# Kernel optimization log

Hardware: AMD Instinct MI355X
Metric: run time of the kernel (lower is better)

Reference implementation:

```python
import jax, jax.numpy as jnp
import numpy as np

L, H, DK, DV, DM, DH = 6, 12, 64, 64, 768, 3072
B, T = 8, 1024


def pos_embed(T, N, dtype):
    pos = jnp.arange(T, dtype=jnp.float32)[:, None]
    i = jnp.arange(N)[None, :]
    exp = ((i // 2) * 2).astype(jnp.float32) / N
    ang = pos / jnp.power(jnp.float32(10000.0), exp)
    pe = jnp.where(i % 2 == 0, jnp.sin(ang), jnp.cos(ang))
    return pe.astype(dtype)


def layernorm(x, g, b, eps=1e-5):
    mu = jnp.mean(x, axis=-1, keepdims=True)
    var = jnp.mean((x - mu) ** 2, axis=-1, keepdims=True)
    return (x - mu) * jax.lax.rsqrt(var + eps) * g + b


def setup_inputs() -> dict:
    key = jax.random.key(0)
    ks = jax.random.split(key, 16)
    s = 0.02
    return {
        "x": jax.random.normal(ks[0], (B, T, DM), dtype=jnp.float32),
        "mask": jnp.ones((B, T), dtype=bool),
        "wq": jax.random.normal(ks[1], (L, H, DM, DK), dtype=jnp.float32) * s,
        "wk": jax.random.normal(ks[2], (L, H, DM, DK), dtype=jnp.float32) * s,
        "wv": jax.random.normal(ks[3], (L, H, DM, DV), dtype=jnp.float32) * s,
        "proj_w": jax.random.normal(ks[4], (L, H * DV, DM), dtype=jnp.float32) * s,
        "proj_b": jnp.zeros((L, DM), dtype=jnp.float32),
        "ln1_g": jnp.ones((L, DM), dtype=jnp.float32),
        "ln1_b": jnp.zeros((L, DM), dtype=jnp.float32),
        "w1": jax.random.normal(ks[5], (L, DM, DH), dtype=jnp.float32) * s,
        "b1": jnp.zeros((L, DH), dtype=jnp.float32),
        "w2": jax.random.normal(ks[6], (L, DH, DM), dtype=jnp.float32) * s,
        "b2": jnp.zeros((L, DM), dtype=jnp.float32),
        "ln2_g": jnp.ones((L, DM), dtype=jnp.float32),
        "ln2_b": jnp.zeros((L, DM), dtype=jnp.float32),
    }


def reference(x, mask, wq, wk, wv, proj_w, proj_b, ln1_g, ln1_b, w1, b1, w2, b2, ln2_g, ln2_b):
    Bx, Tx, Dm = x.shape
    nlayers = wq.shape[0]
    x = x + pos_embed(Tx, Dm, x.dtype)  # sinusoidal PE, added in-place in original
    m = mask[:, None, None, :]          # [B,1,1,Tk], broadcast over heads and queries
    scale = Dm ** 0.5                   # NOTE: original divides by sqrt(Dm), not sqrt(Dk)
    for l in range(nlayers):
        q = jnp.einsum('btd,hdk->bhtk', x, wq[l])
        k = jnp.einsum('bsd,hdk->bhsk', x, wk[l])
        v = jnp.einsum('bsd,hdv->bhsv', x, wv[l])
        attn = jnp.einsum('bhtk,bhsk->bhts', q, k) / scale
        attn = jnp.where(m, attn, -jnp.inf)
        p = jax.nn.softmax(attn, axis=-1)
        o = jnp.einsum('bhts,bhsv->bhtv', p, v)
        o = o.transpose(0, 2, 1, 3).reshape(Bx, Tx, -1)  # concat heads: [B,T,H*Dv]
        o = o @ proj_w[l] + proj_b[l]
        x = layernorm(o + x, ln1_g[l], ln1_b[l])
        h = jax.nn.relu(x @ w1[l] + b1[l])
        f = h @ w2[l] + b2[l]
        x = layernorm(f + x, ln2_g[l], ln2_b[l])
    return x
```

## Files before the change

kernel.cpp:

```cpp
#include <hip/hip_runtime.h>
#include <hip/hip_bf16.h>
#include <math.h>

constexpr int LAYERS = 6;
constexpr int HEADS  = 12;
constexpr int DK     = 64;
constexpr int DM     = 768;
constexpr int DH     = 3072;
constexpr int BATCH  = 8;
constexpr int SEQ    = 1024;
constexpr int MROWS  = BATCH * SEQ;
constexpr float QSCALE = 0.03608439182435161f * 1.4426950408889634f;

typedef __attribute__((ext_vector_type(4))) float f32x4;
typedef __attribute__((ext_vector_type(8))) short bf16x8;
typedef __attribute__((ext_vector_type(4))) unsigned short u16x4;

enum { EPI_QKV = 0, EPI_PROJ = 1, EPI_RELU = 2, EPI_FFN2 = 3 };

__device__ __forceinline__ void gload_lds16(const void* g, void* l) {
  __builtin_amdgcn_global_load_lds(
      (const __attribute__((address_space(1))) void*)g,
      (__attribute__((address_space(3))) void*)l, 16, 0, 0);
}

__global__ __launch_bounds__(256) void posembed_kernel(
    const float* __restrict__ x, __hip_bfloat16* __restrict__ xb) {
  int idx = blockIdx.x * 256 + threadIdx.x;
  int d  = idx % DM;
  int bt = idx / DM;
  int t  = bt & (SEQ - 1);
  float expo = (float)(d & ~1) * (1.0f / (float)DM);
  float inv  = powf(10000.0f, -expo);
  float ang  = (float)t * inv;
  float pe   = (d & 1) ? cosf(ang) : sinf(ang);
  xb[idx] = __float2bfloat16(x[idx] + pe);
}

__global__ __launch_bounds__(256) void transpose_conv(
    const float* __restrict__ in, __hip_bfloat16* __restrict__ out,
    int R, int C, long obatch) {
  __shared__ float tile[32][33];
  int batch = blockIdx.z;
  in  += (long)batch * R * C;
  out += (long)batch * obatch;
  int c0 = blockIdx.x * 32, r0 = blockIdx.y * 32;
  int tx = threadIdx.x, ty = threadIdx.y;
  for (int i = 0; i < 4; i++) {
    int r = r0 + ty + i * 8;
    tile[ty + i * 8][tx] = in[(long)r * C + c0 + tx];
  }
  __syncthreads();
  for (int i = 0; i < 4; i++) {
    int oc = ty + i * 8;
    out[(long)(c0 + oc) * R + r0 + tx] = __float2bfloat16(tile[tx][oc]);
  }
}

__global__ __launch_bounds__(256) void qkv_transpose(
    const float* __restrict__ wq, const float* __restrict__ wk,
    const float* __restrict__ wv, __hip_bfloat16* __restrict__ out) {
  __shared__ float tile[32][33];
  const int z = blockIdx.z;
  const int which = z / 12, head = z % 12;
  const float* in = (which == 0 ? wq : which == 1 ? wk : wv)
                    + (size_t)head * DM * DK;
  __hip_bfloat16* o = out + (size_t)which * DM * DM + (size_t)head * DK * DM;
  int c0 = blockIdx.x * 32, r0 = blockIdx.y * 32;
  int tx = threadIdx.x, ty = threadIdx.y;
  for (int i = 0; i < 4; i++) {
    int r = r0 + ty + i * 8;
    tile[ty + i * 8][tx] = in[(long)r * DK + c0 + tx];
  }
  __syncthreads();
  for (int i = 0; i < 4; i++) {
    int oc = ty + i * 8;
    o[(long)(c0 + oc) * DM + r0 + tx] = __float2bfloat16(tile[tx][oc]);
  }
}

__global__ __launch_bounds__(256) void vtrans_kernel(
    const __hip_bfloat16* __restrict__ v, __hip_bfloat16* __restrict__ vt) {
  __shared__ unsigned short tile[64][66];
  const int head = blockIdx.y;
  const int t0 = blockIdx.x * 64;
  const unsigned short* src =
      (const unsigned short*)v + (size_t)head * SEQ * DK + (size_t)t0 * DK;
  unsigned short* dst = (unsigned short*)vt + (size_t)head * SEQ * DK + t0;
  const int tid = threadIdx.x;
#pragma unroll
  for (int it = 0; it < 4; ++it) {
    int j = tid + it * 256;
    int r = j >> 4;
    int c4 = (j & 15) * 4;
    u16x4 d4 = *(const u16x4*)&src[(size_t)r * DK + c4];
    tile[r][c4 + 0] = d4[0]; tile[r][c4 + 1] = d4[1];
    tile[r][c4 + 2] = d4[2]; tile[r][c4 + 3] = d4[3];
  }
  __syncthreads();
#pragma unroll
  for (int it = 0; it < 4; ++it) {
    int j = tid + it * 256;
    int d = j >> 4;
    int t4 = (j & 15) * 4;
    u16x4 o4;
    o4[0] = tile[t4 + 0][d]; o4[1] = tile[t4 + 1][d];
    o4[2] = tile[t4 + 2][d]; o4[3] = tile[t4 + 3][d];
    *(u16x4*)&dst[(size_t)d * SEQ + t4] = o4;
  }
}

template <int EPI, int BN>
__global__ __launch_bounds__(256, 2) void gemm_bt(
    const __hip_bfloat16* __restrict__ A,
    const __hip_bfloat16* __restrict__ BT,
    int K, int nx,
    const float* __restrict__ bias,
    const __hip_bfloat16* __restrict__ res,
    void* __restrict__ outp) {
  __shared__ __align__(16) char As[2][16384];
  __shared__ __align__(16) char Bs[2][BN * 128];
  constexpr int NF = BN / 32;

  const int nwg = gridDim.x;
  const int cpx = nwg >> 3;
  const int orig = blockIdx.x;
  const int lid = (orig & 7) * cpx + (orig >> 3);
  const int m0 = (lid / nx) * 128;
  const int n0 = (lid % nx) * BN;

  const int tid = threadIdx.x;
  const int lane = tid & 63;
  const int w = tid >> 6;
  const int wm = w >> 1, wn = w & 1;
  const int g = lane >> 4, r16 = lane & 15;
  const int r7 = r16 & 7;

  f32x4 acc[4][NF] = {};

  auto stage = [&](int kt, int d) {
    const int k0 = kt * 64;
#pragma unroll
    for (int i = 0; i < 4; i++) {
      int c = tid + 256 * i;
      int r = c >> 3, cc = (c & 7) ^ (r & 7);
      gload_lds16(&A[(size_t)(m0 + r) * K + k0 + cc * 8], &As[d][c * 16]);
    }
#pragma unroll
    for (int i = 0; i < BN / 32; i++) {
      int c = tid + 256 * i;
      int r = c >> 3, cc = (c & 7) ^ (r & 7);
      gload_lds16(&BT[(size_t)(n0 + r) * K + k0 + cc * 8], &Bs[d][c * 16]);
    }
  };

  const int NT = K >> 6;
  stage(0, 0);
  asm volatile("s_waitcnt vmcnt(0)" ::: "memory");
  __builtin_amdgcn_s_barrier();
  __builtin_amdgcn_sched_barrier(0);

  for (int kt = 0; kt < NT; ++kt) {
    const int cur = kt & 1;
    if (kt + 1 < NT) stage(kt + 1, cur ^ 1);

#pragma unroll
    for (int kk = 0; kk < 2; ++kk) {
      bf16x8 af[4], bfr[NF];
#pragma unroll
      for (int m = 0; m < 4; m++) {
        int R = wm * 64 + m * 16 + r16;
        af[m] = *(const bf16x8*)&As[cur][R * 128 + (((kk * 4 + g) ^ r7) << 4)];
      }
#pragma unroll
      for (int n = 0; n < NF; n++) {
        int R = wn * (BN / 2) + n * 16 + r16;
        bfr[n] = *(const bf16x8*)&Bs[cur][R * 128 + (((kk * 4 + g) ^ r7) << 4)];
      }
      __builtin_amdgcn_s_setprio(1);
#pragma unroll
      for (int m = 0; m < 4; m++)
#pragma unroll
        for (int n = 0; n < NF; n++)
          acc[m][n] = __builtin_amdgcn_mfma_f32_16x16x32_bf16(
              af[m], bfr[n], acc[m][n], 0, 0, 0);
      __builtin_amdgcn_s_setprio(0);
    }

    asm volatile("s_waitcnt vmcnt(0)" ::: "memory");
    __builtin_amdgcn_s_barrier();
    __builtin_amdgcn_sched_barrier(0);
  }

#pragma unroll
  for (int m = 0; m < 4; m++)
#pragma unroll
    for (int n = 0; n < NF; n++)
#pragma unroll
      for (int r = 0; r < 4; r++) {
        int row = m0 + wm * 64 + m * 16 + g * 4 + r;
        int col = n0 + wn * (BN / 2) + n * 16 + r16;
        float v = acc[m][n][r];
        if (EPI == EPI_QKV) {
          int which = (col >= 2 * DM) ? 2 : (col >= DM ? 1 : 0);
          int hc = col - which * DM;
          int h = hc >> 6, dk = hc & 63;
          int b = row >> 10, t = row & (SEQ - 1);
          if (which == 0) v *= QSCALE;
          ((__hip_bfloat16*)outp)[(((size_t)(which * BATCH + b) * HEADS + h) * SEQ + t) * DK + dk] =
              __float2bfloat16(v);
        } else if (EPI == EPI_PROJ || EPI == EPI_FFN2) {
          ((__hip_bfloat16*)outp)[(size_t)row * DM + col] = __float2bfloat16(
              v + bias[col] + __bfloat162float(res[(size_t)row * DM + col]));
        } else {
          v += bias[col];
          ((__hip_bfloat16*)outp)[(size_t)row * DH + col] =
              __float2bfloat16(v > 0.f ? v : 0.f);
        }
      }
}

__global__ __launch_bounds__(256, 4) void flash_kernel(
    const __hip_bfloat16* __restrict__ qkv,
    const __hip_bfloat16* __restrict__ vt,
    __hip_bfloat16* __restrict__ obuf) {
  __shared__ __align__(16) char KL[2][8192];
  __shared__ __align__(16) char VL[2][8192];
  __shared__ __align__(16) char PsL[4][2048];

  const int bid = blockIdx.x;
  const int qb = bid / 96;
  const int bh = bid % 96;
  const int h = bh % HEADS, b = bh / HEADS;

  const int tid = threadIdx.x, lane = tid & 63, w = tid >> 6;
  const int g = lane >> 4, r16 = lane & 15;
  const int r7 = r16 & 7;

  const size_t headoff = ((size_t)b * HEADS + h) * SEQ * DK;
  const size_t planes = (size_t)BATCH * HEADS * SEQ * DK;
  const __hip_bfloat16* Q  = qkv + headoff;
  const __hip_bfloat16* Kg = qkv + planes + headoff;
  const __hip_bfloat16* Vg = vt + headoff;

  bf16x8 qf[2];
  {
    int qrow = qb * 64 + w * 16 + r16;
    qf[0] = *(const bf16x8*)&Q[(size_t)qrow * DK + g * 8];
    qf[1] = *(const bf16x8*)&Q[(size_t)qrow * DK + 32 + g * 8];
  }

  f32x4 o_acc[4] = {};
  float m_run = -3e38f;
  float lsum[4] = {0.f, 0.f, 0.f, 0.f};

  const int s0j = tid, s1j = tid + 256;
  const int s0r = s0j >> 3, s0c = (s0j & 7) ^ (s0r & 7);
  const int s1r = s1j >> 3, s1c = (s1j & 7) ^ (s1r & 7);

  auto stage = [&](int tt, int d) {
    const int ss = tt * 64;
    gload_lds16(&Kg[(size_t)(ss + s0r) * DK + s0c * 8], &KL[d][s0j * 16]);
    gload_lds16(&Kg[(size_t)(ss + s1r) * DK + s1c * 8], &KL[d][s1j * 16]);
    gload_lds16(&Vg[(size_t)s0r * SEQ + ss + s0c * 8], &VL[d][s0j * 16]);
    gload_lds16(&Vg[(size_t)s1r * SEQ + ss + s1c * 8], &VL[d][s1j * 16]);
  };

  stage(0, 0);
  __syncthreads();

  for (int t = 0; t < SEQ / 64; ++t) {
    const int cur = t & 1;
    if (t < SEQ / 64 - 1) stage(t + 1, cur ^ 1);

    f32x4 s_acc[4] = {};
#pragma unroll
    for (int n = 0; n < 4; ++n) {
      const int R = n * 16 + r16;
      bf16x8 k0 = *(const bf16x8*)&KL[cur][R * 128 + ((g ^ r7) << 4)];
      s_acc[n] = __builtin_amdgcn_mfma_f32_16x16x32_bf16(qf[0], k0, s_acc[n], 0, 0, 0);
      bf16x8 k1 = *(const bf16x8*)&KL[cur][R * 128 + (((4 + g) ^ r7) << 4)];
      s_acc[n] = __builtin_amdgcn_mfma_f32_16x16x32_bf16(qf[1], k1, s_acc[n], 0, 0, 0);
    }

    float mx = -3e38f;
#pragma unroll
    for (int n = 0; n < 4; ++n)
      mx = fmaxf(mx, fmaxf(fmaxf(s_acc[n][0], s_acc[n][1]),
                           fmaxf(s_acc[n][2], s_acc[n][3])));
#pragma unroll
    for (int off = 1; off < 16; off <<= 1) mx = fmaxf(mx, __shfl_xor(mx, off, 64));

    if (__any(mx > m_run + 8.f)) {
      float mnew = fmaxf(m_run, mx);
      float alpha = exp2f(m_run - mnew);
      m_run = mnew;
#pragma unroll
      for (int r = 0; r < 4; ++r) lsum[r] *= alpha;
#pragma unroll
      for (int n = 0; n < 4; ++n)
#pragma unroll
        for (int r = 0; r < 4; ++r) o_acc[n][r] *= alpha;
    }

    char* Pw = &PsL[w][0];
#pragma unroll
    for (int n = 0; n < 4; ++n)
#pragma unroll
      for (int r = 0; r < 4; ++r) {
        float p = exp2f(s_acc[n][r] - m_run);
        lsum[r] += p;
        int trow = g * 4 + r;
        int chunk = n * 2 + (r16 >> 3);
        *(unsigned short*)&Pw[trow * 128 + ((chunk * 16) ^ ((trow & 7) << 4)) + r7 * 2] =
            __bfloat16_as_ushort(__float2bfloat16(p));
      }

    asm volatile("s_waitcnt lgkmcnt(0)" ::: "memory");
    __builtin_amdgcn_sched_barrier(0);

#pragma unroll
    for (int kk = 0; kk < 2; ++kk) {
      bf16x8 pf = *(const bf16x8*)&Pw[r16 * 128 + (((kk * 4 + g) * 16) ^ (r7 << 4))];
#pragma unroll
      for (int n = 0; n < 4; ++n) {
        bf16x8 vf = *(const bf16x8*)&VL[cur][(n * 16 + r16) * 128 +
                                            (((kk * 4 + g) ^ r7) << 4)];
        o_acc[n] = __builtin_amdgcn_mfma_f32_16x16x32_bf16(pf, vf, o_acc[n], 0, 0, 0);
      }
    }

    asm volatile("s_waitcnt vmcnt(0)" ::: "memory");
    __builtin_amdgcn_s_barrier();
    __builtin_amdgcn_sched_barrier(0);
  }

#pragma unroll
  for (int r = 0; r < 4; ++r)
#pragma unroll
    for (int off = 1; off < 16; off <<= 1) lsum[r] += __shfl_xor(lsum[r], off, 64);
  float rinv[4];
#pragma unroll
  for (int r = 0; r < 4; ++r) rinv[r] = 1.0f / lsum[r];

#pragma unroll
  for (int n = 0; n < 4; ++n)
#pragma unroll
    for (int r = 0; r < 4; ++r) {
      int t = qb * 64 + w * 16 + g * 4 + r;
      int col = h * DK + n * 16 + r16;
      obuf[((size_t)b * SEQ + t) * DM + col] =
          __float2bfloat16(o_acc[n][r] * rinv[r]);
    }
}

__global__ __launch_bounds__(256) void ln_kernel(
    const __hip_bfloat16* __restrict__ y, const float* __restrict__ gam,
    const float* __restrict__ bet, float* __restrict__ xout,
    __hip_bfloat16* __restrict__ xb) {
  int row = blockIdx.x;
  const __hip_bfloat16* yr = y + (size_t)row * DM;
  int tid = threadIdx.x;
  float v[3];
  float s1 = 0.f, s2 = 0.f;
#pragma unroll
  for (int i = 0; i < 3; i++) {
    v[i] = __bfloat162float(yr[tid + i * 256]);
    s1 += v[i];
    s2 += v[i] * v[i];
  }
#pragma unroll
  for (int off = 1; off < 64; off <<= 1) {
    s1 += __shfl_xor(s1, off, 64);
    s2 += __shfl_xor(s2, off, 64);
  }
  __shared__ float ps1[4], ps2[4];
  int w = tid >> 6;
  if ((tid & 63) == 0) { ps1[w] = s1; ps2[w] = s2; }
  __syncthreads();
  s1 = ps1[0] + ps1[1] + ps1[2] + ps1[3];
  s2 = ps2[0] + ps2[1] + ps2[2] + ps2[3];
  float mu = s1 * (1.f / DM);
  float var = s2 * (1.f / DM) - mu * mu;
  float rstd = rsqrtf(var + 1e-5f);
#pragma unroll
  for (int i = 0; i < 3; i++) {
    int d = tid + i * 256;
    float o = (v[i] - mu) * rstd * gam[d] + bet[d];
    if (xout) xout[(size_t)row * DM + d] = o;
    xb[(size_t)row * DM + d] = __float2bfloat16(o);
  }
}

extern "C" void kernel_launch(void* const* d_in, const int* in_sizes, int n_in,
                              void* d_out, int out_size, void* d_ws, size_t ws_size,
                              hipStream_t stream) {
  const float* x_in   = (const float*)d_in[0];
  const float* wq     = (const float*)d_in[2];
  const float* wk     = (const float*)d_in[3];
  const float* wv     = (const float*)d_in[4];
  const float* proj_w = (const float*)d_in[5];
  const float* proj_b = (const float*)d_in[6];
  const float* ln1_g  = (const float*)d_in[7];
  const float* ln1_b  = (const float*)d_in[8];
  const float* w1     = (const float*)d_in[9];
  const float* b1     = (const float*)d_in[10];
  const float* w2     = (const float*)d_in[11];
  const float* b2     = (const float*)d_in[12];
  const float* ln2_g  = (const float*)d_in[13];
  const float* ln2_b  = (const float*)d_in[14];

  size_t off = 0;
  auto alloc = [&](size_t bytes) {
    void* p = (char*)d_ws + off;
    off += (bytes + 255) & ~(size_t)255;
    return p;
  };
  __hip_bfloat16* xb    = (__hip_bfloat16*)alloc((size_t)MROWS * DM * 2);
  __hip_bfloat16* qkvb  = (__hip_bfloat16*)alloc((size_t)3 * MROWS * DM * 2);
  __hip_bfloat16* obuf  = (__hip_bfloat16*)alloc((size_t)MROWS * DM * 2);
  __hip_bfloat16* ybuf  = (__hip_bfloat16*)alloc((size_t)MROWS * DM * 2);
  __hip_bfloat16* hbuf  = (__hip_bfloat16*)alloc((size_t)MROWS * DH * 2);
  __hip_bfloat16* qkvt  = (__hip_bfloat16*)alloc((size_t)3 * DM * DM * 2);
  __hip_bfloat16* projt = (__hip_bfloat16*)alloc((size_t)DM * DM * 2);
  __hip_bfloat16* w1t   = (__hip_bfloat16*)alloc((size_t)DH * DM * 2);
  __hip_bfloat16* w2t   = (__hip_bfloat16*)alloc((size_t)DM * DH * 2);
  __hip_bfloat16* vtb   = hbuf;

  posembed_kernel<<<MROWS * DM / 256, 256, 0, stream>>>(x_in, xb);

  for (int l = 0; l < LAYERS; l++) {
    qkv_transpose<<<dim3(2, 24, 36), dim3(32, 8), 0, stream>>>(
        wq + (size_t)l * HEADS * DM * DK, wk + (size_t)l * HEADS * DM * DK,
        wv + (size_t)l * HEADS * DM * DK, qkvt);
    transpose_conv<<<dim3(24, 24, 1), dim3(32, 8), 0, stream>>>(
        proj_w + (size_t)l * DM * DM, projt, DM, DM, 0);
    transpose_conv<<<dim3(96, 24, 1), dim3(32, 8), 0, stream>>>(
        w1 + (size_t)l * DM * DH, w1t, DM, DH, 0);
    transpose_conv<<<dim3(24, 96, 1), dim3(32, 8), 0, stream>>>(
        w2 + (size_t)l * DH * DM, w2t, DH, DM, 0);

    gemm_bt<EPI_QKV, 128><<<dim3(18 * 64), 256, 0, stream>>>(
        xb, qkvt, DM, 18, nullptr, nullptr, qkvb);
    vtrans_kernel<<<dim3(16, 96), 256, 0, stream>>>(
        qkvb + (size_t)2 * MROWS * DM, vtb);
    flash_kernel<<<dim3((SEQ / 64) * HEADS * BATCH), 256, 0, stream>>>(
        qkvb, vtb, obuf);
    gemm_bt<EPI_PROJ, 64><<<dim3(64 * 12), 256, 0, stream>>>(
        obuf, projt, DM, 12, proj_b + (size_t)l * DM, xb, ybuf);
    ln_kernel<<<MROWS, 256, 0, stream>>>(
        ybuf, ln1_g + (size_t)l * DM, ln1_b + (size_t)l * DM, nullptr, xb);
    gemm_bt<EPI_RELU, 128><<<dim3(24 * 64), 256, 0, stream>>>(
        xb, w1t, DM, 24, b1 + (size_t)l * DH, nullptr, hbuf);
    gemm_bt<EPI_FFN2, 64><<<dim3(64 * 12), 256, 0, stream>>>(
        hbuf, w2t, DH, 12, b2 + (size_t)l * DM, xb, ybuf);
    float* xo = (l == LAYERS - 1) ? (float*)d_out : nullptr;
    ln_kernel<<<MROWS, 256, 0, stream>>>(
        ybuf, ln2_g + (size_t)l * DM, ln2_b + (size_t)l * DM, xo, xb);
  }
}
```

Baseline: 1.590 ms.

## Fuse V transpose into QKV GEMM epilogue, merge weight transposes, vectorize layernorm

The QKV GEMM epilogue now writes V directly in transposed [b,h,dk,t] layout with packed 4-element stores, which removes the separate vtrans kernel and its extra pass over V. The three fp32-to-bf16 weight transposes per layer are merged into one launch. Layernorm is rewritten to handle one row per wavefront with vectorized loads and stores and no LDS reduction or block barrier. The cost is a more complex epilogue and strided 8-byte stores into V^T.

```diff
diff --git a/kernel.cpp b/kernel.cpp
--- a/kernel.cpp
+++ b/kernel.cpp
@@ -15,6 +15,7 @@
 typedef __attribute__((ext_vector_type(4))) float f32x4;
 typedef __attribute__((ext_vector_type(8))) short bf16x8;
 typedef __attribute__((ext_vector_type(4))) unsigned short u16x4;
+typedef __attribute__((ext_vector_type(8))) unsigned short u16x8;
 
 enum { EPI_QKV = 0, EPI_PROJ = 1, EPI_RELU = 2, EPI_FFN2 = 3 };
 
@@ -22,6 +23,10 @@
   __builtin_amdgcn_global_load_lds(
       (const __attribute__((address_space(1))) void*)g,
       (__attribute__((address_space(3))) void*)l, 16, 0, 0);
+}
+
+__device__ __forceinline__ float bfu2f(unsigned short u) {
+  union { unsigned int i; float f; } c; c.i = (unsigned int)u << 16; return c.f;
 }
 
 __global__ __launch_bounds__(256) void posembed_kernel(
@@ -35,26 +40,6 @@
   float ang  = (float)t * inv;
   float pe   = (d & 1) ? cosf(ang) : sinf(ang);
   xb[idx] = __float2bfloat16(x[idx] + pe);
-}
-
-__global__ __launch_bounds__(256) void transpose_conv(
-    const float* __restrict__ in, __hip_bfloat16* __restrict__ out,
-    int R, int C, long obatch) {
-  __shared__ float tile[32][33];
-  int batch = blockIdx.z;
-  in  += (long)batch * R * C;
-  out += (long)batch * obatch;
-  int c0 = blockIdx.x * 32, r0 = blockIdx.y * 32;
-  int tx = threadIdx.x, ty = threadIdx.y;
-  for (int i = 0; i < 4; i++) {
-    int r = r0 + ty + i * 8;
-    tile[ty + i * 8][tx] = in[(long)r * C + c0 + tx];
-  }
-  __syncthreads();
-  for (int i = 0; i < 4; i++) {
-    int oc = ty + i * 8;
-    out[(long)(c0 + oc) * R + r0 + tx] = __float2bfloat16(tile[tx][oc]);
-  }
 }
 
 __global__ __launch_bounds__(256) void qkv_transpose(
@@ -79,34 +64,29 @@
   }
 }
 
-__global__ __launch_bounds__(256) void vtrans_kernel(
-    const __hip_bfloat16* __restrict__ v, __hip_bfloat16* __restrict__ vt) {
-  __shared__ unsigned short tile[64][66];
-  const int head = blockIdx.y;
-  const int t0 = blockIdx.x * 64;
-  const unsigned short* src =
-      (const unsigned short*)v + (size_t)head * SEQ * DK + (size_t)t0 * DK;
-  unsigned short* dst = (unsigned short*)vt + (size_t)head * SEQ * DK + t0;
-  const int tid = threadIdx.x;
-#pragma unroll
-  for (int it = 0; it < 4; ++it) {
-    int j = tid + it * 256;
-    int r = j >> 4;
-    int c4 = (j & 15) * 4;
-    u16x4 d4 = *(const u16x4*)&src[(size_t)r * DK + c4];
-    tile[r][c4 + 0] = d4[0]; tile[r][c4 + 1] = d4[1];
-    tile[r][c4 + 2] = d4[2]; tile[r][c4 + 3] = d4[3];
+__global__ __launch_bounds__(256) void wtrans_kernel(
+    const float* __restrict__ proj_w, const float* __restrict__ w1,
+    const float* __restrict__ w2, __hip_bfloat16* __restrict__ projt,
+    __hip_bfloat16* __restrict__ w1t, __hip_bfloat16* __restrict__ w2t) {
+  __shared__ float tile[32][33];
+  const int bid = blockIdx.x;
+  const float* in; __hip_bfloat16* out; int R, C, bx, by;
+  if (bid < 576)       { in = proj_w; out = projt; R = DM; C = DM;
+                         bx = bid % 24;          by = bid / 24; }
+  else if (bid < 2880) { int i = bid - 576;  in = w1; out = w1t; R = DM; C = DH;
+                         bx = i % 96;            by = i / 96; }
+  else                 { int i = bid - 2880; in = w2; out = w2t; R = DH; C = DM;
+                         bx = i % 24;            by = i / 24; }
+  const int c0 = bx * 32, r0 = by * 32;
+  const int tx = threadIdx.x, ty = threadIdx.y;
+  for (int i = 0; i < 4; i++) {
+    int r = r0 + ty + i * 8;
+    tile[ty + i * 8][tx] = in[(long)r * C + c0 + tx];
   }
   __syncthreads();
-#pragma unroll
-  for (int it = 0; it < 4; ++it) {
-    int j = tid + it * 256;
-    int d = j >> 4;
-    int t4 = (j & 15) * 4;
-    u16x4 o4;
-    o4[0] = tile[t4 + 0][d]; o4[1] = tile[t4 + 1][d];
-    o4[2] = tile[t4 + 2][d]; o4[3] = tile[t4 + 3][d];
-    *(u16x4*)&dst[(size_t)d * SEQ + t4] = o4;
+  for (int i = 0; i < 4; i++) {
+    int oc = ty + i * 8;
+    out[(long)(c0 + oc) * R + r0 + tx] = __float2bfloat16(tile[tx][oc]);
   }
 }
 
@@ -117,7 +97,7 @@
     int K, int nx,
     const float* __restrict__ bias,
     const __hip_bfloat16* __restrict__ res,
-    void* __restrict__ outp) {
+    void* __restrict__ outp, void* __restrict__ outp2) {
   __shared__ __align__(16) char As[2][16384];
   __shared__ __align__(16) char Bs[2][BN * 128];
   constexpr int NF = BN / 32;
@@ -195,29 +175,47 @@
 #pragma unroll
   for (int m = 0; m < 4; m++)
 #pragma unroll
-    for (int n = 0; n < NF; n++)
-#pragma unroll
-      for (int r = 0; r < 4; r++) {
-        int row = m0 + wm * 64 + m * 16 + g * 4 + r;
-        int col = n0 + wn * (BN / 2) + n * 16 + r16;
-        float v = acc[m][n][r];
-        if (EPI == EPI_QKV) {
-          int which = (col >= 2 * DM) ? 2 : (col >= DM ? 1 : 0);
-          int hc = col - which * DM;
-          int h = hc >> 6, dk = hc & 63;
-          int b = row >> 10, t = row & (SEQ - 1);
-          if (which == 0) v *= QSCALE;
-          ((__hip_bfloat16*)outp)[(((size_t)(which * BATCH + b) * HEADS + h) * SEQ + t) * DK + dk] =
-              __float2bfloat16(v);
-        } else if (EPI == EPI_PROJ || EPI == EPI_FFN2) {
-          ((__hip_bfloat16*)outp)[(size_t)row * DM + col] = __float2bfloat16(
-              v + bias[col] + __bfloat162float(res[(size_t)row * DM + col]));
+    for (int n = 0; n < NF; n++) {
+      const int col = n0 + wn * (BN / 2) + n * 16 + r16;
+      const int row0 = m0 + wm * 64 + m * 16 + g * 4;
+      if (EPI == EPI_QKV) {
+        const int which = (col >= 2 * DM) ? 2 : (col >= DM ? 1 : 0);
+        const int hc = col - which * DM;
+        const int h = hc >> 6, dk = hc & 63;
+        const int b = row0 >> 10, t0 = row0 & (SEQ - 1);
+        if (which == 2) {
+          u16x4 pk;
+#pragma unroll
+          for (int r = 0; r < 4; r++)
+            pk[r] = __bfloat16_as_ushort(__float2bfloat16(acc[m][n][r]));
+          *(u16x4*)&((unsigned short*)outp2)[
+              ((size_t)(b * HEADS + h) * DK + dk) * SEQ + t0] = pk;
         } else {
-          v += bias[col];
-          ((__hip_bfloat16*)outp)[(size_t)row * DH + col] =
+#pragma unroll
+          for (int r = 0; r < 4; r++) {
+            float v = acc[m][n][r];
+            if (which == 0) v *= QSCALE;
+            ((__hip_bfloat16*)outp)[
+                (((size_t)(which * BATCH + b) * HEADS + h) * SEQ + t0 + r) * DK + dk] =
+                __float2bfloat16(v);
+          }
+        }
+      } else if (EPI == EPI_PROJ || EPI == EPI_FFN2) {
+#pragma unroll
+        for (int r = 0; r < 4; r++) {
+          size_t idx = (size_t)(row0 + r) * DM + col;
+          ((__hip_bfloat16*)outp)[idx] = __float2bfloat16(
+              acc[m][n][r] + bias[col] + __bfloat162float(res[idx]));
+        }
+      } else {
+#pragma unroll
+        for (int r = 0; r < 4; r++) {
+          float v = acc[m][n][r] + bias[col];
+          ((__hip_bfloat16*)outp)[(size_t)(row0 + r) * DH + col] =
               __float2bfloat16(v > 0.f ? v : 0.f);
         }
       }
+    }
 }
 
 __global__ __launch_bounds__(256, 4) void flash_kernel(
@@ -358,38 +356,48 @@
     const __hip_bfloat16* __restrict__ y, const float* __restrict__ gam,
     const float* __restrict__ bet, float* __restrict__ xout,
     __hip_bfloat16* __restrict__ xb) {
-  int row = blockIdx.x;
-  const __hip_bfloat16* yr = y + (size_t)row * DM;
-  int tid = threadIdx.x;
-  float v[3];
+  const int wv = threadIdx.x >> 6, lane = threadIdx.x & 63;
+  const int row = blockIdx.x * 4 + wv;
+  const unsigned short* yr = (const unsigned short*)y + (size_t)row * DM;
+
+  u16x8 a = *(const u16x8*)&yr[lane * 8];
+  u16x4 bq = *(const u16x4*)&yr[512 + lane * 4];
+  float v[12];
+#pragma unroll
+  for (int j = 0; j < 8; j++) v[j] = bfu2f(a[j]);
+#pragma unroll
+  for (int j = 0; j < 4; j++) v[8 + j] = bfu2f(bq[j]);
+
   float s1 = 0.f, s2 = 0.f;
 #pragma unroll
-  for (int i = 0; i < 3; i++) {
-    v[i] = __bfloat162float(yr[tid + i * 256]);
-    s1 += v[i];
-    s2 += v[i] * v[i];
-  }
+  for (int j = 0; j < 12; j++) { s1 += v[j]; s2 += v[j] * v[j]; }
 #pragma unroll
   for (int off = 1; off < 64; off <<= 1) {
     s1 += __shfl_xor(s1, off, 64);
     s2 += __shfl_xor(s2, off, 64);
   }
-  __shared__ float ps1[4], ps2[4];
-  int w = tid >> 6;
-  if ((tid & 63) == 0) { ps1[w] = s1; ps2[w] = s2; }
-  __syncthreads();
-  s1 = ps1[0] + ps1[1] + ps1[2] + ps1[3];
-  s2 = ps2[0] + ps2[1] + ps2[2] + ps2[3];
   float mu = s1 * (1.f / DM);
   float var = s2 * (1.f / DM) - mu * mu;
   float rstd = rsqrtf(var + 1e-5f);
-#pragma unroll
-  for (int i = 0; i < 3; i++) {
-    int d = tid + i * 256;
-    float o = (v[i] - mu) * rstd * gam[d] + bet[d];
+
+  u16x8 oa; u16x4 ob;
+#pragma unroll
+  for (int j = 0; j < 8; j++) {
+    int d = lane * 8 + j;
+    float o = (v[j] - mu) * rstd * gam[d] + bet[d];
     if (xout) xout[(size_t)row * DM + d] = o;
-    xb[(size_t)row * DM + d] = __float2bfloat16(o);
-  }
+    oa[j] = __bfloat16_as_ushort(__float2bfloat16(o));
+  }
+#pragma unroll
+  for (int j = 0; j < 4; j++) {
+    int d = 512 + lane * 4 + j;
+    float o = (v[8 + j] - mu) * rstd * gam[d] + bet[d];
+    if (xout) xout[(size_t)row * DM + d] = o;
+    ob[j] = __bfloat16_as_ushort(__float2bfloat16(o));
+  }
+  unsigned short* xr = (unsigned short*)xb + (size_t)row * DM;
+  *(u16x8*)&xr[lane * 8] = oa;
+  *(u16x4*)&xr[512 + lane * 4] = ob;
 }
 
 extern "C" void kernel_launch(void* const* d_in, const int* in_sizes, int n_in,
@@ -417,7 +425,7 @@
     return p;
   };
   __hip_bfloat16* xb    = (__hip_bfloat16*)alloc((size_t)MROWS * DM * 2);
-  __hip_bfloat16* qkvb  = (__hip_bfloat16*)alloc((size_t)3 * MROWS * DM * 2);
+  __hip_bfloat16* qkvb  = (__hip_bfloat16*)alloc((size_t)2 * MROWS * DM * 2);
   __hip_bfloat16* obuf  = (__hip_bfloat16*)alloc((size_t)MROWS * DM * 2);
   __hip_bfloat16* ybuf  = (__hip_bfloat16*)alloc((size_t)MROWS * DM * 2);
   __hip_bfloat16* hbuf  = (__hip_bfloat16*)alloc((size_t)MROWS * DH * 2);
@@ -433,29 +441,24 @@
     qkv_transpose<<<dim3(2, 24, 36), dim3(32, 8), 0, stream>>>(
         wq + (size_t)l * HEADS * DM * DK, wk + (size_t)l * HEADS * DM * DK,
         wv + (size_t)l * HEADS * DM * DK, qkvt);
-    transpose_conv<<<dim3(24, 24, 1), dim3(32, 8), 0, stream>>>(
-        proj_w + (size_t)l * DM * DM, projt, DM, DM, 0);
-    transpose_conv<<<dim3(96, 24, 1), dim3(32, 8), 0, stream>>>(
-        w1 + (size_t)l * DM * DH, w1t, DM, DH, 0);
-    transpose_conv<<<dim3(24, 96, 1), dim3(32, 8), 0, stream>>>(
-        w2 + (size_t)l * DH * DM, w2t, DH, DM, 0);
+    wtrans_kernel<<<dim3(5184), dim3(32, 8), 0, stream>>>(
+        proj_w + (size_t)l * DM * DM, w1 + (size_t)l * DM * DH,
+        w2 + (size_t)l * DH * DM, projt, w1t, w2t);
 
     gemm_bt<EPI_QKV, 128><<<dim3(18 * 64), 256, 0, stream>>>(
-        xb, qkvt, DM, 18, nullptr, nullptr, qkvb);
-    vtrans_kernel<<<dim3(16, 96), 256, 0, stream>>>(
-        qkvb + (size_t)2 * MROWS * DM, vtb);
+        xb, qkvt, DM, 18, nullptr, nullptr, qkvb, vtb);
     flash_kernel<<<dim3((SEQ / 64) * HEADS * BATCH), 256, 0, stream>>>(
         qkvb, vtb, obuf);
     gemm_bt<EPI_PROJ, 64><<<dim3(64 * 12), 256, 0, stream>>>(
-        obuf, projt, DM, 12, proj_b + (size_t)l * DM, xb, ybuf);
-    ln_kernel<<<MROWS, 256, 0, stream>>>(
+        obuf, projt, DM, 12, proj_b + (size_t)l * DM, xb, ybuf, nullptr);
+    ln_kernel<<<MROWS / 4, 256, 0, stream>>>(
         ybuf, ln1_g + (size_t)l * DM, ln1_b + (size_t)l * DM, nullptr, xb);
     gemm_bt<EPI_RELU, 128><<<dim3(24 * 64), 256, 0, stream>>>(
-        xb, w1t, DM, 24, b1 + (size_t)l * DH, nullptr, hbuf);
+        xb, w1t, DM, 24, b1 + (size_t)l * DH, nullptr, hbuf, nullptr);
     gemm_bt<EPI_FFN2, 64><<<dim3(64 * 12), 256, 0, stream>>>(
-        hbuf, w2t, DH, 12, b2 + (size_t)l * DM, xb, ybuf);
+        hbuf, w2t, DH, 12, b2 + (size_t)l * DM, xb, ybuf, nullptr);
     float* xo = (l == LAYERS - 1) ? (float*)d_out : nullptr;
-    ln_kernel<<<MROWS, 256, 0, stream>>>(
+    ln_kernel<<<MROWS / 4, 256, 0, stream>>>(
         ybuf, ln2_g + (size_t)l * DM, ln2_b + (size_t)l * DM, xo, xb);
   }
 }
```

New measurement: 1.704 ms. 7.2% more time.
